# Performance work log

Measured on AMD Instinct MI355X. Metric: run time of the kernel, lower is better.

The kernel has to match this reference:

```python
import jax, jax.numpy as jnp
import numpy as np

BIN_SIZE = 20
OFFSET = 1.0


def setup_inputs() -> dict:
    key = jax.random.key(0)
    k1, k2 = jax.random.split(key)
    latents = jax.random.normal(k1, (32, 256, 16, 16), dtype=jnp.float32)
    time_steps = jax.random.randint(k2, (32,), 0, 4096, dtype=jnp.int32)
    return {"latents": latents, "time_steps": time_steps}


def reference(latents, time_steps):
    # latents: [B, L, H, W], time_steps: [B] int
    B, L, H, W = latents.shape
    # 'exp' normalization buffer: norm[i] = 2^((i+1)/bs) - 2^(i/bs), mean-normalized
    i = jnp.arange(L, dtype=jnp.float32)
    norm = jnp.exp2((i + 1.0) / BIN_SIZE) - jnp.exp2(i / BIN_SIZE)
    norm = norm / jnp.mean(norm)
    # per-channel weight applied inside each ragged slice: norm[L-1] / norm[k]
    w = norm[L - 1] / norm  # [L]

    ts = time_steps.astype(jnp.float32)
    dt = jnp.abs(ts[None, :] - ts[:, None]) + OFFSET  # [B, B]
    bins = jnp.clip(jnp.ceil(jnp.log2(dt) * BIN_SIZE), 0, L).astype(jnp.int32)  # [B, B] in [0, L]

    # per-pair, per-channel L1 summed over spatial dims: D[i, j, k] = sum_hw |x[j,k] - x[i,k]|
    D = jnp.sum(jnp.abs(latents[None, :] - latents[:, None]), axis=(3, 4))  # [B, B, L]
    Wd = D * w  # weighted channel contributions

    # ragged suffix-sum via zero-padded cumsum: dist[i,j] = sum_{k >= bins[i,j]} Wd[i,j,k]
    # bins == L naturally yields 0 (the i==j / out-of-range case)
    csp = jnp.concatenate([jnp.zeros((B, B, 1), Wd.dtype), jnp.cumsum(Wd, axis=2)], axis=2)  # [B, B, L+1]
    prefix = jnp.take_along_axis(csp, bins[..., None], axis=2)[..., 0]
    distances = csp[..., -1] - prefix  # [B, B]

    return jnp.mean(distances)  # reduction='mean'
```

## Files before the change

kernel.cpp:

```cpp
#include <hip/hip_runtime.h>

constexpr int BSZ  = 32;
constexpr int LCH  = 256;
constexpr int NPAIRS = (BSZ * (BSZ - 1)) / 2;
constexpr int NQ   = 4;
constexpr int PQ   = NPAIRS / NQ;
constexpr int NBLK = LCH * NQ;

typedef unsigned long long u64;
constexpr unsigned MAGIC = 0x5AD0C0DEu;


__device__ __forceinline__ constexpr int pair_idx(int i, int j) {
    return 30 * i - (i * (i - 1)) / 2 + j - 1;
}

template <int BASE>
__device__ __forceinline__ void accum_q(const float* __restrict__ x,
                                        const unsigned* __restrict__ m,
                                        float* __restrict__ acc) {
#pragma unroll
    for (int w = 0; w < 4; ++w) {
        if (m[w] == 0u) continue;
#pragma unroll
        for (int i = 0; i < BSZ - 1; ++i) {
#pragma unroll
            for (int j = i + 1; j < BSZ; ++j) {
                const int p = pair_idx(i, j);
                if (p >= BASE && p < BASE + PQ && ((p - BASE) >> 5) == w) {
                    const int b = p - BASE;
                    const float g = ((m[w] >> (b & 31)) & 1u) ? 1.0f : 0.0f;
                    acc[b & 3] = fmaf(g, fabsf(x[i] - x[j]), acc[b & 3]);
                }
            }
        }
    }
}

__global__ __launch_bounds__(256) void ts_one_kernel(
    const float* __restrict__ latents,
    const int*   __restrict__ ts,
    u64*         __restrict__ slots,
    float*       __restrict__ out)
{
    const int blk = blockIdx.x;
    const int k   = blk >> 2;
    const int q   = blk & 3;
    const int tid = threadIdx.x;

    __shared__ unsigned lm[4];

    bool act = false;
    if (tid < PQ) {
        const int p = q * PQ + tid;
        int i = 0, s = 0;
        while (s + (31 - i) <= p) { s += 31 - i; ++i; }
        const int j = i + 1 + (p - s);
        const float dt = fabsf((float)(ts[j] - ts[i])) + 1.0f;
        int bins = (int)ceilf(log2f(dt) * 20.0f);
        bins = min(max(bins, 0), LCH);
        act = (bins <= k);
    }
    const unsigned long long bal = __ballot(act);
    if (tid == 0)       { lm[0] = (unsigned)bal; lm[1] = (unsigned)(bal >> 32); }
    else if (tid == 64) { lm[2] = (unsigned)bal; lm[3] = (unsigned)(bal >> 32); }
    __syncthreads();

    unsigned m[4];
#pragma unroll
    for (int c = 0; c < 4; ++c)
        m[c] = __builtin_amdgcn_readfirstlane(lm[c]);

    float res = 0.0f;
    if ((m[0] | m[1] | m[2] | m[3]) != 0u) {
        float x[BSZ];
#pragma unroll
        for (int b = 0; b < BSZ; ++b)
            x[b] = latents[((size_t)b << 16) + ((size_t)k << 8) + (size_t)tid];

        float acc[4] = {0.0f, 0.0f, 0.0f, 0.0f};
        switch (q) {
            case 0: accum_q<0>(x, m, acc);      break;
            case 1: accum_q<PQ>(x, m, acc);     break;
            case 2: accum_q<2 * PQ>(x, m, acc); break;
            default: accum_q<3 * PQ>(x, m, acc); break;
        }
        res = (acc[0] + acc[1]) + (acc[2] + acc[3]);

        for (int off = 32; off > 0; off >>= 1)
            res += __shfl_down(res, off, 64);
        __shared__ float wsum[4];
        if ((tid & 63) == 0) wsum[tid >> 6] = res;
        __syncthreads();
        res = (wsum[0] + wsum[1]) + (wsum[2] + wsum[3]);
    }

    if (tid == 0) {
        const float wk = exp2f((float)(LCH - 1 - k) * 0.05f);
        const unsigned bits = __float_as_uint(res * wk);
        const u64 v = ((u64)MAGIC << 32) | (u64)bits;
        __hip_atomic_store(&slots[blk], v, __ATOMIC_RELAXED,
                           __HIP_MEMORY_SCOPE_AGENT);
    }

    if (blk != 0) return;

    double s = 0.0;
#pragma unroll
    for (int r = 0; r < NBLK / 256; ++r) {
        const int idx = tid + 256 * r;
        u64 v;
        do {
            v = __hip_atomic_load(&slots[idx], __ATOMIC_RELAXED,
                                  __HIP_MEMORY_SCOPE_AGENT);
        } while ((unsigned)(v >> 32) != MAGIC);
        s += (double)__uint_as_float((unsigned)v);
    }
    for (int off = 32; off > 0; off >>= 1)
        s += __shfl_down(s, off, 64);
    __shared__ double ds[4];
    if ((tid & 63) == 0) ds[tid >> 6] = s;
    __syncthreads();
    if (tid == 0)
        out[0] = (float)(((ds[0] + ds[1]) + (ds[2] + ds[3])) * (2.0 / 1024.0));
}

extern "C" void kernel_launch(void* const* d_in, const int* in_sizes, int n_in,
                              void* d_out, int out_size, void* d_ws, size_t ws_size,
                              hipStream_t stream)
{
    const float* latents = (const float*)d_in[0];
    const int*   ts      = (const int*)d_in[1];
    float*       out     = (float*)d_out;
    u64*         slots   = (u64*)d_ws;

    ts_one_kernel<<<NBLK, 256, 0, stream>>>(latents, ts, slots, out);
}
```

Before: 10.40 us.

## Merge four pair-quarter blocks per channel into one 1024-thread block

New measurement: 12.71 us. +22.2%, slower.

```diff
diff --git a/kernel.cpp b/kernel.cpp
--- a/kernel.cpp
+++ b/kernel.cpp
@@ -5,7 +5,7 @@
 constexpr int NPAIRS = (BSZ * (BSZ - 1)) / 2;
 constexpr int NQ   = 4;
 constexpr int PQ   = NPAIRS / NQ;
-constexpr int NBLK = LCH * NQ;
+constexpr int NBLK = LCH;
 
 typedef unsigned long long u64;
 constexpr unsigned MAGIC = 0x5AD0C0DEu;
@@ -37,22 +37,23 @@
     }
 }
 
-__global__ __launch_bounds__(256) void ts_one_kernel(
+__global__ __launch_bounds__(1024) void ts_chan_kernel(
     const float* __restrict__ latents,
     const int*   __restrict__ ts,
     u64*         __restrict__ slots,
     float*       __restrict__ out)
 {
-    const int blk = blockIdx.x;
-    const int k   = blk >> 2;
-    const int q   = blk & 3;
-    const int tid = threadIdx.x;
+    const int k    = blockIdx.x;
+    const int tid  = threadIdx.x;
+    const int site = tid & 255;
+    const int q    = tid >> 8;
+    const int sub  = (tid >> 6) & 3;
 
-    __shared__ unsigned lm[4];
+    __shared__ unsigned lm[16];
 
     bool act = false;
-    if (tid < PQ) {
-        const int p = q * PQ + tid;
+    if (sub < 2 && site < PQ) {
+        const int p = q * PQ + site;
         int i = 0, s = 0;
         while (s + (31 - i) <= p) { s += 31 - i; ++i; }
         const int j = i + 1 + (p - s);
@@ -62,21 +63,23 @@
         act = (bins <= k);
     }
     const unsigned long long bal = __ballot(act);
-    if (tid == 0)       { lm[0] = (unsigned)bal; lm[1] = (unsigned)(bal >> 32); }
-    else if (tid == 64) { lm[2] = (unsigned)bal; lm[3] = (unsigned)(bal >> 32); }
+    if (sub < 2 && (tid & 63) == 0) {
+        lm[q * 4 + sub * 2]     = (unsigned)bal;
+        lm[q * 4 + sub * 2 + 1] = (unsigned)(bal >> 32);
+    }
     __syncthreads();
 
     unsigned m[4];
 #pragma unroll
     for (int c = 0; c < 4; ++c)
-        m[c] = __builtin_amdgcn_readfirstlane(lm[c]);
+        m[c] = __builtin_amdgcn_readfirstlane(lm[q * 4 + c]);
 
     float res = 0.0f;
     if ((m[0] | m[1] | m[2] | m[3]) != 0u) {
         float x[BSZ];
 #pragma unroll
         for (int b = 0; b < BSZ; ++b)
-            x[b] = latents[((size_t)b << 16) + ((size_t)k << 8) + (size_t)tid];
+            x[b] = latents[((size_t)b << 16) + ((size_t)k << 8) + (size_t)site];
 
         float acc[4] = {0.0f, 0.0f, 0.0f, 0.0f};
         switch (q) {
@@ -86,43 +89,45 @@
             default: accum_q<3 * PQ>(x, m, acc); break;
         }
         res = (acc[0] + acc[1]) + (acc[2] + acc[3]);
-
-        for (int off = 32; off > 0; off >>= 1)
-            res += __shfl_down(res, off, 64);
-        __shared__ float wsum[4];
-        if ((tid & 63) == 0) wsum[tid >> 6] = res;
-        __syncthreads();
-        res = (wsum[0] + wsum[1]) + (wsum[2] + wsum[3]);
     }
 
+    for (int off = 32; off > 0; off >>= 1)
+        res += __shfl_down(res, off, 64);
+    __shared__ float wsum[16];
+    if ((tid & 63) == 0) wsum[tid >> 6] = res;
+    __syncthreads();
     if (tid == 0) {
+        float t = 0.0f;
+#pragma unroll
+        for (int w = 0; w < 16; ++w) t += wsum[w];
         const float wk = exp2f((float)(LCH - 1 - k) * 0.05f);
-        const unsigned bits = __float_as_uint(res * wk);
-        const u64 v = ((u64)MAGIC << 32) | (u64)bits;
-        __hip_atomic_store(&slots[blk], v, __ATOMIC_RELAXED,
-                           __HIP_MEMORY_SCOPE_AGENT);
+        const unsigned bits = __float_as_uint(t * wk);
+        __hip_atomic_store(&slots[k], ((u64)MAGIC << 32) | (u64)bits,
+                           __ATOMIC_RELAXED, __HIP_MEMORY_SCOPE_AGENT);
     }
 
-    if (blk != 0) return;
+    if (k != 0) return;
 
     double s = 0.0;
-#pragma unroll
-    for (int r = 0; r < NBLK / 256; ++r) {
-        const int idx = tid + 256 * r;
+    if (tid < LCH) {
         u64 v;
         do {
-            v = __hip_atomic_load(&slots[idx], __ATOMIC_RELAXED,
+            v = __hip_atomic_load(&slots[tid], __ATOMIC_RELAXED,
                                   __HIP_MEMORY_SCOPE_AGENT);
         } while ((unsigned)(v >> 32) != MAGIC);
-        s += (double)__uint_as_float((unsigned)v);
+        s = (double)__uint_as_float((unsigned)v);
     }
     for (int off = 32; off > 0; off >>= 1)
         s += __shfl_down(s, off, 64);
-    __shared__ double ds[4];
+    __shared__ double ds[16];
     if ((tid & 63) == 0) ds[tid >> 6] = s;
     __syncthreads();
-    if (tid == 0)
-        out[0] = (float)(((ds[0] + ds[1]) + (ds[2] + ds[3])) * (2.0 / 1024.0));
+    if (tid == 0) {
+        double t = 0.0;
+#pragma unroll
+        for (int w = 0; w < 16; ++w) t += ds[w];
+        out[0] = (float)(t * (2.0 / 1024.0));
+    }
 }
 
 extern "C" void kernel_launch(void* const* d_in, const int* in_sizes, int n_in,
@@ -134,5 +139,5 @@
     float*       out     = (float*)d_out;
     u64*         slots   = (u64*)d_ws;
 
-    ts_one_kernel<<<NBLK, 256, 0, stream>>>(latents, ts, slots, out);
+    ts_chan_kernel<<<NBLK, 1024, 0, stream>>>(latents, ts, slots, out);
 }
```
